# Kernel tuning notes

Hardware: AMD Instinct MI355X
Metric: run time of the kernel (lower is better)

Reference implementation:

```python
import jax, jax.numpy as jnp
import numpy as np

KERNEL_SIGMA2 = 4096.0  # = 2 * x_dim, assumed Gaussian RBF kernel

B, K, D, H, Z = 512, 32, 2048, 512, 64


def setup_inputs() -> dict:
    key = jax.random.key(0)
    ks = jax.random.split(key, 8)
    s = lambda k, shp, fan: jax.random.normal(k, shp, jnp.float32) / np.sqrt(fan)
    return {
        "x_c": jax.random.normal(ks[0], (B, D), jnp.float32),
        "x_nn": jax.random.normal(ks[1], (B, K, D), jnp.float32),
        "W1": s(ks[2], (D, H), D), "b1": jnp.zeros((H,), jnp.float32),
        "W2": s(ks[3], (H, Z), H), "b2": jnp.zeros((Z,), jnp.float32),
        "V1": s(ks[4], (Z, H), Z), "c1": jnp.zeros((H,), jnp.float32),
        "V2": s(ks[5], (H, D), H), "c2": jnp.zeros((D,), jnp.float32),
    }


def _enc(x, W1, b1, W2, b2):
    return jax.nn.relu(x @ W1 + b1) @ W2 + b2


def _dec(z, V1, c1, V2, c2):
    return jax.nn.relu(z @ V1 + c1) @ V2 + c2


def reference(x_c, x_nn, W1, b1, W2, b2, V1, c1, V2, c2):
    bs, num_nn, x_dim = x_nn.shape
    z_c = _enc(x_c, W1, b1, W2, b2)                       # [B, Z]
    z_dim = z_c.shape[1]
    z_nn = _enc(x_nn.reshape(bs * num_nn, x_dim), W1, b1, W2, b2)
    z_nn = z_nn.reshape(bs, num_nn, z_dim)
    dz = z_nn - z_c[:, None, :]                           # [B, K, Z]

    # first-order Taylor: recon(z_c) + J(z_c) @ dz via JVP of decoder
    dec_fn = lambda z: _dec(z, V1, c1, V2, c2)
    inputs = jnp.broadcast_to(z_c[:, None, :], (bs, num_nn, z_dim)).reshape(-1, z_dim)
    _, Jdz = jax.jvp(dec_fn, (inputs,), (dz.reshape(-1, z_dim),))  # [B*K, D]

    recon = dec_fn(z_c)                                   # [B, D]
    n_recon = recon[:, None, :] + Jdz.reshape(bs, num_nn, x_dim)

    diff = x_nn - n_recon
    n_loss = jnp.sum(diff * diff, axis=2)                 # ||.||^2, [B, K]
    w = jnp.exp(-jnp.sum((x_nn - x_c[:, None, :]) ** 2, axis=2) / KERNEL_SIGMA2)
    return jnp.mean(w * n_loss)
```

## Files before the change

kernel.cpp:

```cpp
#include <hip/hip_runtime.h>
#include <hip/hip_bf16.h>
#include <cstdint>
#include <cstddef>

#define DEV __device__ __forceinline__

typedef __bf16 bf16;
typedef __bf16 bf16x8 __attribute__((ext_vector_type(8)));
typedef float f32x4 __attribute__((ext_vector_type(4)));

DEV f32x4 mfma16(bf16x8 a, bf16x8 b, f32x4 c) {
  return __builtin_amdgcn_mfma_f32_16x16x32_bf16(a, b, c, 0, 0, 0);
}

DEV void glds16(const void* g, void* l) {
  __builtin_amdgcn_global_load_lds(
      (const __attribute__((address_space(1))) void*)g,
      (__attribute__((address_space(3))) void*)l, 16, 0, 0);
}

template<int ROWS, int NT>
DEV void stage_tile(const bf16* __restrict__ src, int ld, int row0, int k0,
                    unsigned char* lds, int tid) {
  constexpr int CALLS = (ROWS * 128) / (NT * 16);
  const int wid = tid >> 6, lane = tid & 63;
#pragma unroll
  for (int c = 0; c < CALLS; ++c) {
    const int obase = c * (NT * 16) + wid * 1024;
    const int o = obase + lane * 16;
    const int row = o >> 7;
    const int scb = (o & 127) ^ ((row & 7) << 4);
    glds16(src + (size_t)(row0 + row) * ld + k0 + (scb >> 1), lds + obase);
  }
}

template<int ROWS, int NT>
DEV void stage_tile_f32(const float* __restrict__ src, int ld, int row0, int k0,
                        unsigned char* lds, int tid) {
  constexpr int CALLS = (ROWS * 256) / (NT * 16);
  const int wid = tid >> 6, lane = tid & 63;
#pragma unroll
  for (int c = 0; c < CALLS; ++c) {
    const int obase = c * (NT * 16) + wid * 1024;
    const int o = obase + lane * 16;
    const int row = o >> 8;
    const int scb = (o & 255) ^ ((row & 7) << 4);
    glds16(src + (size_t)(row0 + row) * ld + k0 + (scb >> 2), lds + obase);
  }
}

template<int BM, int BN, int WM, int WN, int MODE, int AF32, int MINW = 2>
__global__ __launch_bounds__(WM*WN*64, MINW) void gemm_kernel(
    const bf16* __restrict__ A, const float* __restrict__ Af,
    const float* __restrict__ Af2,
    const bf16* __restrict__ Bt, const float* __restrict__ bias,
    int M, int N, int K,
    float* __restrict__ out32, bf16* __restrict__ out16,
    const float* __restrict__ hc, const float* __restrict__ recon,
    float* __restrict__ nloss, float* __restrict__ warg)
{
  constexpr int NT = WM * WN * 64;
  constexpr int FM = (BM / WM) / 16;
  constexpr int FN = (BN / WN) / 16;
  __shared__ __align__(16) unsigned char smem[AF32 ? (BM * 256 + BN * 128)
                                                   : (BM + BN) * 128];

  const int tid = threadIdx.x, lane = tid & 63, wid = tid >> 6;
  const int wm = wid / WN, wn = wid % WN;
  const int wm0 = wm * (BM / WM), wn0 = wn * (BN / WN);

  int bx = blockIdx.x, by = blockIdx.y;
  {
    const int gx = gridDim.x;
    const int nwg = gx * gridDim.y;
    if ((nwg & 7) == 0) {
      const int fid = by * gx + bx;
      const int cpx = nwg >> 3;
      const int w = (fid & 7) * cpx + (fid >> 3);
      bx = w % gx; by = w / gx;
    }
  }
  const int i0 = by * BM, j0 = bx * BN;
  const int l15 = lane & 15, lg = lane >> 4;

  f32x4 acc[FM][FN] = {};

  int arow[FM], brow[FN];
#pragma unroll
  for (int mi = 0; mi < FM; ++mi) arow[mi] = wm0 + mi * 16 + l15;
#pragma unroll
  for (int ni = 0; ni < FN; ++ni) brow[ni] = wn0 + ni * 16 + l15;

  auto compute = [&](const unsigned char* cA, const unsigned char* cB) {
#pragma unroll
    for (int kh = 0; kh < 2; ++kh) {
      bf16x8 af[FM], bfr[FN];
      if constexpr (AF32) {
        const int Fb = kh * 128 + lg * 32;
#pragma unroll
        for (int mi = 0; mi < FM; ++mi) {
          const int r = arow[mi];
          const unsigned char* p = cA + r * 256;
          const f32x4 lo = *reinterpret_cast<const f32x4*>(p + ((Fb)      ^ ((r & 7) << 4)));
          const f32x4 hi = *reinterpret_cast<const f32x4*>(p + ((Fb + 16) ^ ((r & 7) << 4)));
          bf16x8 a;
          a[0] = (bf16)lo[0]; a[1] = (bf16)lo[1]; a[2] = (bf16)lo[2]; a[3] = (bf16)lo[3];
          a[4] = (bf16)hi[0]; a[5] = (bf16)hi[1]; a[6] = (bf16)hi[2]; a[7] = (bf16)hi[3];
          af[mi] = a;
        }
      } else {
        const int koff = kh * 64 + lg * 16;
#pragma unroll
        for (int mi = 0; mi < FM; ++mi) {
          const int off = (arow[mi] * 128 + koff) ^ ((arow[mi] & 7) << 4);
          af[mi] = *reinterpret_cast<const bf16x8*>(cA + off);
        }
      }
      const int koffB = kh * 64 + lg * 16;
#pragma unroll
      for (int ni = 0; ni < FN; ++ni) {
        const int off = (brow[ni] * 128 + koffB) ^ ((brow[ni] & 7) << 4);
        bfr[ni] = *reinterpret_cast<const bf16x8*>(cB + off);
      }
#pragma unroll
      for (int mi = 0; mi < FM; ++mi)
#pragma unroll
        for (int ni = 0; ni < FN; ++ni)
          acc[mi][ni] = mfma16(af[mi], bfr[ni], acc[mi][ni]);
    }
  };

  if constexpr (AF32) {
    const float* As = (i0 < 512) ? Af + (size_t)i0 * K
                                 : Af2 + (size_t)(i0 - 512) * K;
    for (int kt = 0; kt < K; kt += 64) {
      stage_tile_f32<BM, NT>(As, K, 0, kt, smem, tid);
      stage_tile<BN, NT>(Bt, K, j0, kt, smem + BM * 256, tid);
      __syncthreads();
      compute(smem, smem + BM * 256);
      __syncthreads();
    }
  } else {
    for (int kt = 0; kt < K; kt += 64) {
      stage_tile<BM, NT>(A, K, i0, kt, smem, tid);
      stage_tile<BN, NT>(Bt, K, j0, kt, smem + BM * 128, tid);
      __syncthreads();
      compute(smem, smem + BM * 128);
      __syncthreads();
    }
  }

  if constexpr (MODE == 5) {
    float* eb = (float*)smem;
#pragma unroll
    for (int mi = 0; mi < FM; ++mi) {
      __syncthreads();
#pragma unroll
      for (int ni = 0; ni < FN; ++ni) {
        const int col = wn0 + ni * 16 + l15;
        const int lr0 = wm * 16 + lg * 4;
#pragma unroll
        for (int r = 0; r < 4; ++r)
          eb[(lr0 + r) * 132 + col] = acc[mi][ni][r];
      }
      __syncthreads();
      const int lrow = tid >> 3;
      const int c0 = (tid & 7) * 16;
      const int grow = i0 + (lrow >> 4) * 64 + mi * 16 + (lrow & 15);
      const int b = grow >> 5;
      const float* xp = Af2  + (size_t)grow * 2048 + j0 + c0;
      const float* cp = Af   + (size_t)b * 2048 + j0 + c0;
      const float* rp = recon + (size_t)b * 2048 + j0 + c0;
      float nl = 0.f, wa = 0.f;
#pragma unroll
      for (int q4 = 0; q4 < 4; ++q4) {
        const float4 xv = *(const float4*)(xp + q4 * 4);
        const float4 cv = *(const float4*)(cp + q4 * 4);
        const float4 rv = *(const float4*)(rp + q4 * 4);
#pragma unroll
        for (int q = 0; q < 4; ++q) {
          const float xf = ((const float*)&xv)[q];
          const float d = xf - ((const float*)&rv)[q] - eb[lrow * 132 + c0 + q4 * 4 + q];
          nl += d * d;
          const float wd = xf - ((const float*)&cv)[q];
          wa += wd * wd;
        }
      }
      nl += __shfl_xor(nl, 1, 64); wa += __shfl_xor(wa, 1, 64);
      nl += __shfl_xor(nl, 2, 64); wa += __shfl_xor(wa, 2, 64);
      nl += __shfl_xor(nl, 4, 64); wa += __shfl_xor(wa, 4, 64);
      if ((tid & 7) == 0) {
        atomicAdd(&nloss[grow], nl);
        atomicAdd(&warg[grow], wa);
      }
    }
  } else {
#pragma unroll
    for (int mi = 0; mi < FM; ++mi) {
#pragma unroll
      for (int ni = 0; ni < FN; ++ni) {
#pragma unroll
        for (int r = 0; r < 4; ++r) {
          const int row = i0 + wm0 + mi * 16 + lg * 4 + r;
          const int col = j0 + wn0 + ni * 16 + l15;
          float v = acc[mi][ni][r];
          if constexpr (MODE == 0) {
            v += bias[col];
            out16[(size_t)row * N + col] = (bf16)fmaxf(v, 0.f);
          } else if constexpr (MODE == 1) {
            v += bias[col];
            out32[(size_t)row * N + col] = v;
          } else if constexpr (MODE == 2) {
            v += bias[col];
            out32[(size_t)row * N + col] = v;
            out16[(size_t)row * N + col] = (bf16)fmaxf(v, 0.f);
          } else if constexpr (MODE == 4) {
            const int b = row >> 5;
            const float m = hc[(size_t)b * 512 + col];
            out16[(size_t)row * N + col] = (bf16)(m > 0.f ? v : 0.f);
          }
        }
      }
    }
  }
}

__global__ void transpose_all_kernel(
    const float* __restrict__ W1, const float* __restrict__ W2,
    const float* __restrict__ V1, const float* __restrict__ V2,
    bf16* __restrict__ W1t, bf16* __restrict__ W2t,
    bf16* __restrict__ V1t, bf16* __restrict__ V2t) {
  int blk = blockIdx.x;
  const float* src; bf16* dst; int R, C, gx;
  if (blk < 1024)      { src = W1; dst = W1t; R = 2048; C = 512;  gx = 16; }
  else if (blk < 1056) { blk -= 1024; src = W2; dst = W2t; R = 512; C = 64;   gx = 2;  }
  else if (blk < 1088) { blk -= 1056; src = V1; dst = V1t; R = 64;  C = 512;  gx = 16; }
  else                 { blk -= 1088; src = V2; dst = V2t; R = 512; C = 2048; gx = 64; }
  __shared__ float t[32][33];
  const int c0 = (blk % gx) * 32, r0 = (blk / gx) * 32;
  const int tx = threadIdx.x, ty = threadIdx.y;
#pragma unroll
  for (int i = 0; i < 32; i += 8)
    t[ty + i][tx] = src[(size_t)(r0 + ty + i) * C + c0 + tx];
  __syncthreads();
#pragma unroll
  for (int i = 0; i < 32; i += 8)
    dst[(size_t)(c0 + ty + i) * R + r0 + tx] = (bf16)t[tx][ty + i];
}

__global__ void dz_prep_kernel(const float* __restrict__ z,
                               bf16* __restrict__ dzb,
                               bf16* __restrict__ zcb,
                               float* __restrict__ nw,
                               float* __restrict__ out) {
  const int i = blockIdx.x * 256 + threadIdx.x;
  if (i < 32768) nw[i] = 0.f;
  if (i == 0) out[0] = 0.f;
  const int r = i >> 6, j = i & 63;
  const float v = z[i];
  if (r < 512) {
    zcb[i] = (bf16)v;
  } else {
    const int rn = r - 512;
    const int b = rn >> 5;
    dzb[(size_t)rn * 64 + j] = (bf16)(v - z[(size_t)b * 64 + j]);
  }
}

__global__ void finalize_kernel(const float* __restrict__ nloss,
                                const float* __restrict__ warg,
                                float* __restrict__ out) {
  const int i = blockIdx.x * 256 + threadIdx.x;
  float v = expf(-warg[i] * (1.0f / 4096.0f)) * nloss[i] * (1.0f / 16384.0f);
#pragma unroll
  for (int s = 1; s < 64; s <<= 1) v += __shfl_xor(v, s, 64);
  __shared__ float red[4];
  const int lane = threadIdx.x & 63, w = threadIdx.x >> 6;
  if (lane == 0) red[w] = v;
  __syncthreads();
  if (threadIdx.x == 0) atomicAdd(out, red[0] + red[1] + red[2] + red[3]);
}

extern "C" void kernel_launch(void* const* d_in, const int* in_sizes, int n_in,
                              void* d_out, int out_size, void* d_ws, size_t ws_size,
                              hipStream_t stream) {
  const float* x_c = (const float*)d_in[0];
  const float* x_nn = (const float*)d_in[1];
  const float* W1 = (const float*)d_in[2];
  const float* b1 = (const float*)d_in[3];
  const float* W2 = (const float*)d_in[4];
  const float* b2 = (const float*)d_in[5];
  const float* V1 = (const float*)d_in[6];
  const float* c1 = (const float*)d_in[7];
  const float* V2 = (const float*)d_in[8];
  const float* c2 = (const float*)d_in[9];
  float* out = (float*)d_out;
  char* ws = (char*)d_ws;

  size_t off = 0;
  auto take = [&](size_t n) { size_t o = off; off += n; return o; };
  bf16*  W1t   = (bf16*) (ws + take((size_t)512 * 2048 * 2));
  bf16*  W2t   = (bf16*) (ws + take((size_t)64 * 512 * 2));
  bf16*  V1t   = (bf16*) (ws + take((size_t)512 * 64 * 2));
  bf16*  V2t   = (bf16*) (ws + take((size_t)2048 * 512 * 2));
  bf16*  h1    = (bf16*) (ws + take((size_t)16896 * 512 * 2));
  float* z     = (float*)(ws + take((size_t)16896 * 64 * 4));
  bf16*  dzb   = (bf16*) (ws + take((size_t)16384 * 64 * 2));
  bf16*  zcb   = (bf16*) (ws + take((size_t)512 * 64 * 2));
  float* hc    = (float*)(ws + take((size_t)512 * 512 * 4));
  bf16*  acb   = (bf16*) (ws + take((size_t)512 * 512 * 2));
  float* recon = (float*)(ws + take((size_t)512 * 2048 * 4));
  bf16*  dab   = (bf16*) (ws + take((size_t)16384 * 512 * 2));
  float* nloss = (float*)(ws + take((size_t)16384 * 4));
  float* warg  = (float*)(ws + take((size_t)16384 * 4));

  transpose_all_kernel<<<dim3(2112), dim3(32, 8), 0, stream>>>(
      W1, W2, V1, V2, W1t, W2t, V1t, V2t);

  gemm_kernel<128, 128, 2, 2, 0, 1, 1><<<dim3(4, 132), dim3(256), 0, stream>>>(
      nullptr, x_c, x_nn, W1t, b1, 16896, 512, 2048,
      nullptr, h1, nullptr, nullptr, nullptr, nullptr);

  gemm_kernel<64, 64, 2, 2, 1, 0><<<dim3(1, 264), dim3(256), 0, stream>>>(
      h1, nullptr, nullptr, W2t, b2, 16896, 64, 512,
      z, nullptr, nullptr, nullptr, nullptr, nullptr);

  dz_prep_kernel<<<dim3(4224), dim3(256), 0, stream>>>(z, dzb, zcb, nloss, out);

  gemm_kernel<128, 128, 2, 2, 2, 0><<<dim3(4, 4), dim3(256), 0, stream>>>(
      zcb, nullptr, nullptr, V1t, c1, 512, 512, 64,
      hc, acb, nullptr, nullptr, nullptr, nullptr);

  gemm_kernel<64, 128, 2, 2, 1, 0><<<dim3(16, 8), dim3(256), 0, stream>>>(
      acb, nullptr, nullptr, V2t, c2, 512, 2048, 512,
      recon, nullptr, nullptr, nullptr, nullptr, nullptr);

  gemm_kernel<128, 128, 2, 2, 4, 0><<<dim3(4, 128), dim3(256), 0, stream>>>(
      dzb, nullptr, nullptr, V1t, nullptr, 16384, 512, 64,
      nullptr, dab, hc, nullptr, nullptr, nullptr);

  gemm_kernel<128, 128, 2, 2, 5, 0><<<dim3(16, 128), dim3(256), 0, stream>>>(
      dab, x_c, x_nn, V2t, nullptr, 16384, 2048, 512,
      nullptr, nullptr, nullptr, recon, nloss, warg);

  finalize_kernel<<<dim3(64), dim3(256), 0, stream>>>(nloss, warg, out);
}
```

Baseline: 163.7 us.

## Load B fragments directly to registers with prefetch in fp32-A GEMM path

In the fp32-A GEMM path, the B tile is no longer staged through LDS; each wave loads its B fragments straight from global memory into registers, one k-tile ahead, double-buffered in registers. This cuts LDS footprint and LDS traffic for B and overlaps the B global loads with compute. The cost is more register pressure, which may lower occupancy. It also drops the coalesced staged loads in favour of per-lane 16-byte global reads, and waves that share B columns now each fetch those columns separately.

```diff
diff --git a/kernel.cpp b/kernel.cpp
--- a/kernel.cpp
+++ b/kernel.cpp
@@ -62,7 +62,7 @@
   constexpr int NT = WM * WN * 64;
   constexpr int FM = (BM / WM) / 16;
   constexpr int FN = (BN / WN) / 16;
-  __shared__ __align__(16) unsigned char smem[AF32 ? (BM * 256 + BN * 128)
+  __shared__ __align__(16) unsigned char smem[AF32 ? (BM * 256)
                                                    : (BM + BN) * 128];
 
   const int tid = threadIdx.x, lane = tid & 63, wid = tid >> 6;
@@ -94,9 +94,44 @@
   auto compute = [&](const unsigned char* cA, const unsigned char* cB) {
 #pragma unroll
     for (int kh = 0; kh < 2; ++kh) {
+      const int koff = kh * 64 + lg * 16;
       bf16x8 af[FM], bfr[FN];
-      if constexpr (AF32) {
+#pragma unroll
+      for (int mi = 0; mi < FM; ++mi) {
+        const int off = (arow[mi] * 128 + koff) ^ ((arow[mi] & 7) << 4);
+        af[mi] = *reinterpret_cast<const bf16x8*>(cA + off);
+      }
+#pragma unroll
+      for (int ni = 0; ni < FN; ++ni) {
+        const int off = (brow[ni] * 128 + koff) ^ ((brow[ni] & 7) << 4);
+        bfr[ni] = *reinterpret_cast<const bf16x8*>(cB + off);
+      }
+#pragma unroll
+      for (int mi = 0; mi < FM; ++mi)
+#pragma unroll
+        for (int ni = 0; ni < FN; ++ni)
+          acc[mi][ni] = mfma16(af[mi], bfr[ni], acc[mi][ni]);
+    }
+  };
+
+  if constexpr (AF32) {
+    const float* As = (i0 < 512) ? Af + (size_t)i0 * K
+                                 : Af2 + (size_t)(i0 - 512) * K;
+    bf16x8 breg[2][FN], bnxt[2][FN];
+
+    auto loadB = [&](bf16x8 (&br)[2][FN], int kt) {
+#pragma unroll
+      for (int kh = 0; kh < 2; ++kh)
+#pragma unroll
+        for (int ni = 0; ni < FN; ++ni)
+          br[kh][ni] = *reinterpret_cast<const bf16x8*>(
+              Bt + (size_t)(j0 + brow[ni]) * K + kt + kh * 32 + lg * 8);
+    };
+    auto computeA32 = [&](const unsigned char* cA, bf16x8 (&br)[2][FN]) {
+#pragma unroll
+      for (int kh = 0; kh < 2; ++kh) {
         const int Fb = kh * 128 + lg * 32;
+        bf16x8 af[FM];
 #pragma unroll
         for (int mi = 0; mi < FM; ++mi) {
           const int r = arow[mi];
@@ -108,37 +143,26 @@
           a[4] = (bf16)hi[0]; a[5] = (bf16)hi[1]; a[6] = (bf16)hi[2]; a[7] = (bf16)hi[3];
           af[mi] = a;
         }
-      } else {
-        const int koff = kh * 64 + lg * 16;
-#pragma unroll
-        for (int mi = 0; mi < FM; ++mi) {
-          const int off = (arow[mi] * 128 + koff) ^ ((arow[mi] & 7) << 4);
-          af[mi] = *reinterpret_cast<const bf16x8*>(cA + off);
-        }
-      }
-      const int koffB = kh * 64 + lg * 16;
-#pragma unroll
-      for (int ni = 0; ni < FN; ++ni) {
-        const int off = (brow[ni] * 128 + koffB) ^ ((brow[ni] & 7) << 4);
-        bfr[ni] = *reinterpret_cast<const bf16x8*>(cB + off);
-      }
-#pragma unroll
-      for (int mi = 0; mi < FM; ++mi)
-#pragma unroll
-        for (int ni = 0; ni < FN; ++ni)
-          acc[mi][ni] = mfma16(af[mi], bfr[ni], acc[mi][ni]);
-    }
-  };
-
-  if constexpr (AF32) {
-    const float* As = (i0 < 512) ? Af + (size_t)i0 * K
-                                 : Af2 + (size_t)(i0 - 512) * K;
+#pragma unroll
+        for (int mi = 0; mi < FM; ++mi)
+#pragma unroll
+          for (int ni = 0; ni < FN; ++ni)
+            acc[mi][ni] = mfma16(af[mi], br[kh][ni], acc[mi][ni]);
+      }
+    };
+
+    loadB(breg, 0);
     for (int kt = 0; kt < K; kt += 64) {
       stage_tile_f32<BM, NT>(As, K, 0, kt, smem, tid);
-      stage_tile<BN, NT>(Bt, K, j0, kt, smem + BM * 256, tid);
-      __syncthreads();
-      compute(smem, smem + BM * 256);
-      __syncthreads();
+      if (kt + 64 < K) loadB(bnxt, kt + 64);
+      __syncthreads();
+      computeA32(smem, breg);
+      __syncthreads();
+#pragma unroll
+      for (int kh = 0; kh < 2; ++kh)
+#pragma unroll
+        for (int ni = 0; ni < FN; ++ni)
+          breg[kh][ni] = bnxt[kh][ni];
     }
   } else {
     for (int kt = 0; kt < K; kt += 64) {
```

Measured after the change: 238.0 us. 45.4% more time.
